# Kernel tuning notes

Measured on AMD Instinct MI355X. Metric: run time of the kernel, lower is better.

The kernel has to match this reference:

```python
import jax, jax.numpy as jnp
import numpy as np

HIDDEN = 768
NUM_HEADS = 12
HEAD_DIM = HIDDEN // NUM_HEADS
B, S = 4, 2048


def setup_inputs() -> dict:
    key = jax.random.key(0)
    ks = jax.random.split(key, 10)
    scale = 1.0 / np.sqrt(HIDDEN)
    return {
        "hidden_states": jax.random.normal(ks[0], (B, S, HIDDEN), dtype=jnp.float32),
        "attention_mask": jnp.ones((B, S), dtype=jnp.float32),
        "Wq": jax.random.normal(ks[1], (HIDDEN, HIDDEN), dtype=jnp.float32) * scale,
        "bq": jnp.zeros((HIDDEN,), dtype=jnp.float32),
        "Wk": jax.random.normal(ks[2], (HIDDEN, HIDDEN), dtype=jnp.float32) * scale,
        "bk": jnp.zeros((HIDDEN,), dtype=jnp.float32),
        "Wv": jax.random.normal(ks[3], (HIDDEN, HIDDEN), dtype=jnp.float32) * scale,
        "bv": jnp.zeros((HIDDEN,), dtype=jnp.float32),
        "Wo": jax.random.normal(ks[4], (HIDDEN, HIDDEN), dtype=jnp.float32) * scale,
        "bo": jnp.zeros((HIDDEN,), dtype=jnp.float32),
    }


def reference(hidden_states, attention_mask, Wq, bq, Wk, bk, Wv, bv, Wo, bo):
    b, s, _ = hidden_states.shape
    # nn.Linear: x @ W.T + b  (W is [out, in])
    Q = hidden_states @ Wq.T + bq
    K = hidden_states @ Wk.T + bk
    V = hidden_states @ Wv.T + bv
    # [b, s, h*d] -> [b, h, s, d]
    Q = Q.reshape(b, s, NUM_HEADS, HEAD_DIM).transpose(0, 2, 1, 3)
    K = K.reshape(b, s, NUM_HEADS, HEAD_DIM).transpose(0, 2, 1, 3)
    V = V.reshape(b, s, NUM_HEADS, HEAD_DIM).transpose(0, 2, 1, 3)
    # scores: [b, h, s, s]
    scores = jnp.einsum("bhqd,bhkd->bhqk", Q, K) / jnp.sqrt(
        jnp.asarray(HEAD_DIM, dtype=Q.dtype))
    # mask: [b, s] -> additive bias broadcast over heads and query dim
    bias = (1.0 - attention_mask)[:, None, None, :] * -10000.0
    scores = scores + bias
    probs = jax.nn.softmax(scores, axis=-1)  # dropout p=0.0 -> identity
    context = jnp.einsum("bhqk,bhkd->bhqd", probs, V)
    context = context.transpose(0, 2, 1, 3).reshape(b, s, HIDDEN)
    return context @ Wo.T + bo
```

## Files before the change

### kernel.cpp

```cpp
#include <hip/hip_runtime.h>
#include <hip/hip_bf16.h>

#define SEQ   2048
#define NH    12
#define MTOK  8192

typedef __attribute__((ext_vector_type(8))) short short8;
typedef __attribute__((ext_vector_type(4))) short short4v;
typedef __attribute__((ext_vector_type(4))) float f32x4;

__device__ inline short f2bf(float x) {
  __hip_bfloat16 h = __float2bfloat16(x);
  return *(short*)&h;
}

#define GLL(gp, lp) __builtin_amdgcn_global_load_lds( \
    (const __attribute__((address_space(1))) void*)(gp), \
    (__attribute__((address_space(3))) void*)(lp), 16, 0, 0)

#define MFMA(a, b, c) __builtin_amdgcn_mfma_f32_16x16x32_bf16(a, b, c, 0, 0, 0)

#if !defined(__HIP_DEVICE_COMPILE__)
#define MFMA16(a, b, c) (c)
#elif __has_builtin(__builtin_amdgcn_mfma_f32_16x16x16bf16_1k)
#define MFMA16(a, b, c) __builtin_amdgcn_mfma_f32_16x16x16bf16_1k(a, b, c, 0, 0, 0)
#elif __has_builtin(__builtin_amdgcn_mfma_f32_16x16x16_bf16)
#define MFMA16(a, b, c) __builtin_amdgcn_mfma_f32_16x16x16_bf16(a, b, c, 0, 0, 0)
#else
#error "no 16x16x16 bf16 mfma builtin on device"
#endif

#if !defined(__HIP_DEVICE_COMPILE__)
#define EXP2(x) (x)
#elif __has_builtin(__builtin_amdgcn_exp2f)
#define EXP2(x) __builtin_amdgcn_exp2f(x)
#else
#define EXP2(x) __expf((x) * 0.6931471805599453f)
#endif

__device__ inline unsigned pack2bf(float a, float b) {
  unsigned ua = __float_as_uint(a) + 0x8000u;
  unsigned ub = __float_as_uint(b) + 0x8000u;
#if defined(__HIP_DEVICE_COMPILE__) && __has_builtin(__builtin_amdgcn_perm)
  return __builtin_amdgcn_perm(ub, ua, 0x07060302u);
#else
  return (ub & 0xFFFF0000u) | (ua >> 16);
#endif
}

union PackFrag {
  unsigned u[2];
  short4v s;
};

#define QSCALE 0.18033688011112042f
#define MBSCALE -14426.950408889634f

__global__ __launch_bounds__(256) void prep(
    const float* __restrict__ hs, const float* __restrict__ Wq,
    const float* __restrict__ Wk, const float* __restrict__ Wv,
    const float* __restrict__ Wo, const float* __restrict__ mask,
    short* __restrict__ Xb, short* __restrict__ Wqkvb,
    short* __restrict__ Wob, float* __restrict__ mbias) {
  int bid = blockIdx.x;
  if (bid < 6144) {
    int i = bid * 256 + threadIdx.x;
    float4 v = ((const float4*)hs)[i];
    short4v o;
    o[0] = f2bf(v.x); o[1] = f2bf(v.y); o[2] = f2bf(v.z); o[3] = f2bf(v.w);
    ((short4v*)Xb)[i] = o;
  } else if (bid < 6144 + 2304) {
    int idx = (bid - 6144) * 256 + threadIdx.x;
    int r = idx / 192, c = (idx - r * 192) * 4;
    const float* src;
    short* dst;
    int rr;
    if (r < 768)       { src = Wq; rr = r;        dst = Wqkvb; }
    else if (r < 1536) { src = Wk; rr = r - 768;  dst = Wqkvb; }
    else if (r < 2304) { src = Wv; rr = r - 1536; dst = Wqkvb; }
    else               { src = Wo; rr = r - 2304; dst = Wob; r = rr; }
    float4 v = *(const float4*)&src[(size_t)rr * 768 + c];
    short4v o;
    o[0] = f2bf(v.x); o[1] = f2bf(v.y); o[2] = f2bf(v.z); o[3] = f2bf(v.w);
    *(short4v*)&dst[(size_t)r * 768 + c] = o;
  } else {
    int i = (bid - 6144 - 2304) * 256 + threadIdx.x;
    if (i < MTOK) mbias[i] = (1.f - mask[i]) * MBSCALE;
  }
}

#define GEMM_BK64_LOOP(Aptr, Bptr)                                            \
  __shared__ __align__(16) short As[128 * 64];                                \
  __shared__ __align__(16) short Bs[128 * 64];                                \
  const int t = threadIdx.x;                                                  \
  const int wid = t >> 6, lane = t & 63, l15 = lane & 15, quad = lane >> 4;   \
  const int bm = blockIdx.x * 128, bn = blockIdx.y * 128;                     \
  const int mq = (wid & 1) * 64, nq = (wid >> 1) * 64;                        \
  const int srow8 = lane >> 3;                                                \
  const int schunk = lane & 7;                                                \
  const int scol = (schunk ^ srow8) * 8;                                      \
  f32x4 acc[4][4] = {};                                                       \
  const short *gA[4], *gB[4];                                                 \
  _Pragma("unroll") for (int g = 0; g < 4; ++g) {                             \
    int row = wid * 32 + g * 8 + srow8;                                       \
    gA[g] = (Aptr) + (size_t)(bm + row) * 768 + scol;                         \
    gB[g] = (Bptr) + (size_t)(bn + row) * 768 + scol;                         \
  }                                                                           \
  for (int k0 = 0; k0 < 768; k0 += 64) {                                      \
    _Pragma("unroll") for (int g = 0; g < 4; ++g)                             \
      GLL(gA[g] + k0, &As[(wid * 32 + g * 8) * 64]);                          \
    _Pragma("unroll") for (int g = 0; g < 4; ++g)                             \
      GLL(gB[g] + k0, &Bs[(wid * 32 + g * 8) * 64]);                          \
    __syncthreads();                                                          \
    _Pragma("unroll") for (int ks = 0; ks < 2; ++ks) {                        \
      short8 a[4], b[4];                                                      \
      _Pragma("unroll") for (int mt = 0; mt < 4; ++mt)                        \
        a[mt] = *(const short8*)&As[(mq + mt * 16 + l15) * 64 +               \
                                    (((ks * 4 + quad) ^ (l15 & 7)) * 8)];     \
      _Pragma("unroll") for (int nt = 0; nt < 4; ++nt)                        \
        b[nt] = *(const short8*)&Bs[(nq + nt * 16 + l15) * 64 +               \
                                    (((ks * 4 + quad) ^ (l15 & 7)) * 8)];     \
      _Pragma("unroll") for (int mt = 0; mt < 4; ++mt)                        \
        _Pragma("unroll") for (int nt = 0; nt < 4; ++nt)                      \
          acc[mt][nt] = MFMA(a[mt], b[nt], acc[mt][nt]);                      \
    }                                                                         \
    __syncthreads();                                                          \
  }

__global__ __launch_bounds__(256) void gemm_qkv(
    const short* __restrict__ A, const short* __restrict__ B,
    const float* __restrict__ bq, const float* __restrict__ bk,
    const float* __restrict__ bv, short* __restrict__ Qb,
    short* __restrict__ Kb, short* __restrict__ Vt) {
  GEMM_BK64_LOOP(A, B)

  const int seg = bn >= 1536 ? 2 : (bn >= 768 ? 1 : 0);
  const float* bias = seg == 0 ? bq : (seg == 1 ? bk : bv);
  const int colbase = bn - seg * 768;

  if (seg < 2) {
    short* dst = seg == 0 ? Qb : Kb;
    const float sc = seg == 0 ? QSCALE : 1.f;
#pragma unroll
    for (int mt = 0; mt < 4; ++mt)
#pragma unroll
      for (int nt = 0; nt < 4; ++nt) {
        int col = colbase + nq + nt * 16 + l15;
        float bias_v = bias[col];
#pragma unroll
        for (int i = 0; i < 4; ++i) {
          int row = bm + mq + mt * 16 + quad * 4 + i;
          dst[(size_t)row * 768 + col] = f2bf((acc[mt][nt][i] + bias_v) * sc);
        }
      }
  } else {
#pragma unroll
    for (int mt = 0; mt < 4; ++mt) {
      int row0 = bm + mq + mt * 16 + quad * 4;
      int b_ = row0 >> 11, s = row0 & 2047;
#pragma unroll
      for (int nt = 0; nt < 4; ++nt) {
        int col = colbase + nq + nt * 16 + l15;
        float bias_v = bias[col];
        int h = col >> 6, d = col & 63;
        short4v pv;
#pragma unroll
        for (int i = 0; i < 4; ++i) pv[i] = f2bf(acc[mt][nt][i] + bias_v);
        *(short4v*)&Vt[(((size_t)b_ * NH + h) * 64 + d) * 2048 + s] = pv;
      }
    }
  }
}

__global__ __launch_bounds__(256) void gemm_out(
    const short* __restrict__ A, const short* __restrict__ B,
    const float* __restrict__ bias, float* __restrict__ C) {
  GEMM_BK64_LOOP(A, B)

#pragma unroll
  for (int mt = 0; mt < 4; ++mt)
#pragma unroll
    for (int nt = 0; nt < 4; ++nt) {
      int col = bn + nq + nt * 16 + l15;
      float bias_v = bias[col];
#pragma unroll
      for (int i = 0; i < 4; ++i) {
        int row = bm + mq + mt * 16 + quad * 4 + i;
        C[(size_t)row * 768 + col] = acc[mt][nt][i] + bias_v;
      }
    }
}

__global__ __launch_bounds__(256, 3) void attn_v8(
    const short* __restrict__ Qb, const short* __restrict__ Kb,
    const short* __restrict__ Vt, const float* __restrict__ maskb,
    short* __restrict__ Ctx) {
  __shared__ __align__(16) short Ks[2][64 * 64];
  __shared__ __align__(16) short Vs[2][64 * 64];
  const int t = threadIdx.x;
  const int w = t >> 6, lane = t & 63, l15 = lane & 15, quad = lane >> 4;
  const int bh = blockIdx.x, b = bh / NH, h = bh % NH;
  const int q0 = blockIdx.y * 128;

  short8 qa[2][2];
#pragma unroll
  for (int qt = 0; qt < 2; ++qt)
#pragma unroll
    for (int ks = 0; ks < 2; ++ks) {
      int row = b * 2048 + q0 + w * 32 + qt * 16 + l15;
      qa[qt][ks] = *(const short8*)&Qb[(size_t)row * 768 + h * 64 + ks * 32 + quad * 8];
    }

  f32x4 O[2][4] = {};
  f32x4 lacc[2] = {};
  short4v ones4;
#pragma unroll
  for (int j = 0; j < 4; ++j) ones4[j] = (short)0x3F80;

  const int r0 = w * 16 + (lane >> 3);
  const int pc = lane & 7;
  const int swz0 = (pc ^ (r0 & 7)) * 8;
  const int swz1 = (pc ^ ((r0 + 8) & 7)) * 8;
  const short* gK0 = Kb + (size_t)(b * 2048 + r0) * 768 + h * 64 + swz0;
  const short* gK1 = Kb + (size_t)(b * 2048 + r0 + 8) * 768 + h * 64 + swz1;
  const short* gV0 = Vt + ((size_t)bh * 64 + r0) * 2048 + swz0;
  const short* gV1 = Vt + ((size_t)bh * 64 + r0 + 8) * 2048 + swz1;
  const float* mb = maskb + b * 2048;
  const int rs = l15 & 7;

  GLL(gK0, &Ks[0][(w * 16) * 64]);
  GLL(gK1, &Ks[0][(w * 16 + 8) * 64]);
  GLL(gV0, &Vs[0][(w * 16) * 64]);
  GLL(gV1, &Vs[0][(w * 16 + 8) * 64]);

  for (int ti = 0; ti < 32; ++ti) {
    const int cur = ti & 1;
    const int k0 = ti * 64;
    __syncthreads();

    {
      const size_t kn = (size_t)(((ti + 1) & 31) * 64);
      GLL(gK0 + kn * 768, &Ks[1 - cur][(w * 16) * 64]);
      GLL(gK1 + kn * 768, &Ks[1 - cur][(w * 16 + 8) * 64]);
      GLL(gV0 + kn, &Vs[1 - cur][(w * 16) * 64]);
      GLL(gV1 + kn, &Vs[1 - cur][(w * 16 + 8) * 64]);
    }

    f32x4 S[4][2] = {};
#pragma unroll
    for (int ks = 0; ks < 2; ++ks) {
      short8 kb[4];
#pragma unroll
      for (int kt = 0; kt < 4; ++kt)
        kb[kt] = *(const short8*)&Ks[cur][(kt * 16 + l15) * 64 +
                                         (((ks * 4 + quad) ^ rs) * 8)];
#pragma unroll
      for (int kt = 0; kt < 4; ++kt) {
        S[kt][0] = MFMA(kb[kt], qa[0][ks], S[kt][0]);
        S[kt][1] = MFMA(kb[kt], qa[1][ks], S[kt][1]);
      }
    }

    short4v pb[4][2];
#pragma unroll
    for (int kt = 0; kt < 4; ++kt) {
      float4 mb4 = *(const float4*)&mb[k0 + kt * 16 + quad * 4];
#pragma unroll
      for (int qt = 0; qt < 2; ++qt) {
        float p0 = EXP2(S[kt][qt][0] + mb4.x);
        float p1 = EXP2(S[kt][qt][1] + mb4.y);
        float p2 = EXP2(S[kt][qt][2] + mb4.z);
        float p3 = EXP2(S[kt][qt][3] + mb4.w);
        PackFrag pf;
        pf.u[0] = pack2bf(p0, p1);
        pf.u[1] = pack2bf(p2, p3);
        pb[kt][qt] = pf.s;
      }
    }

#pragma unroll
    for (int kt = 0; kt < 4; ++kt) {
      lacc[0] = MFMA16(ones4, pb[kt][0], lacc[0]);
      lacc[1] = MFMA16(ones4, pb[kt][1], lacc[1]);
    }

#pragma unroll
    for (int kt = 0; kt < 4; ++kt) {
#pragma unroll
      for (int dt = 0; dt < 4; ++dt) {
        short4v av = *(const short4v*)&Vs[cur][(dt * 16 + l15) * 64 +
            (((kt * 2 + (quad >> 1)) ^ rs) * 8) + (quad & 1) * 4];
        O[0][dt] = MFMA16(av, pb[kt][0], O[0][dt]);
        O[1][dt] = MFMA16(av, pb[kt][1], O[1][dt]);
      }
    }
  }

#pragma unroll
  for (int qt = 0; qt < 2; ++qt) {
    float inv = 1.f / lacc[qt][0];
    int row = b * 2048 + q0 + w * 32 + qt * 16 + l15;
#pragma unroll
    for (int dt = 0; dt < 4; ++dt) {
      PackFrag pf;
      pf.u[0] = pack2bf(O[qt][dt][0] * inv, O[qt][dt][1] * inv);
      pf.u[1] = pack2bf(O[qt][dt][2] * inv, O[qt][dt][3] * inv);
      *(short4v*)&Ctx[(size_t)row * 768 + h * 64 + dt * 16 + quad * 4] = pf.s;
    }
  }
}

extern "C" void kernel_launch(void* const* d_in, const int* in_sizes, int n_in,
                              void* d_out, int out_size, void* d_ws,
                              size_t ws_size, hipStream_t stream) {
  const float* hs   = (const float*)d_in[0];
  const float* mask = (const float*)d_in[1];
  const float* Wq   = (const float*)d_in[2];
  const float* bq   = (const float*)d_in[3];
  const float* Wk   = (const float*)d_in[4];
  const float* bk   = (const float*)d_in[5];
  const float* Wv   = (const float*)d_in[6];
  const float* bv   = (const float*)d_in[7];
  const float* Wo   = (const float*)d_in[8];
  const float* bo   = (const float*)d_in[9];

  char* ws = (char*)d_ws;
  short* Xb    = (short*)(ws);
  short* Wqkvb = (short*)(ws + 12582912);
  short* Wob   = (short*)(ws + 16121856);
  short* Qb    = (short*)(ws + 17301504);
  short* Kb    = (short*)(ws + 29884416);
  short* Vtg   = (short*)(ws + 42467328);
  short* Ctxb  = (short*)(ws + 55050240);
  float* mbias = (float*)(ws + 67633152);

  prep<<<8480, 256, 0, stream>>>(hs, Wq, Wk, Wv, Wo, mask,
                                 Xb, Wqkvb, Wob, mbias);
  gemm_qkv<<<dim3(64, 18), 256, 0, stream>>>(Xb, Wqkvb, bq, bk, bv,
                                             Qb, Kb, Vtg);
  attn_v8<<<dim3(48, 16), 256, 0, stream>>>(Qb, Kb, Vtg, mbias, Ctxb);
  gemm_out<<<dim3(64, 6), 256, 0, stream>>>(Ctxb, Wob, bo, (float*)d_out);
}
```

Before: 229.6 us.

## Split attention block into 8 waves of 16 query rows each

Attention blocks now launch 8 waves of 512 threads. Each wave handles 16 query rows instead of 32, and each thread loads one K and one V row chunk per tile instead of two. This halves per-thread registers and work so more waves can fit per CU and hide latency. In exchange, K/V fragments read from LDS are reused across fewer query rows, so LDS read traffic per unit of MFMA work doubles.

```diff
diff --git a/kernel.cpp b/kernel.cpp
--- a/kernel.cpp
+++ b/kernel.cpp
@@ -191,7 +191,7 @@
     }
 }
 
-__global__ __launch_bounds__(256, 3) void attn_v8(
+__global__ __launch_bounds__(512, 6) void attn_v9(
     const short* __restrict__ Qb, const short* __restrict__ Kb,
     const short* __restrict__ Vt, const float* __restrict__ maskb,
     short* __restrict__ Ctx) {
@@ -202,36 +202,29 @@
   const int bh = blockIdx.x, b = bh / NH, h = bh % NH;
   const int q0 = blockIdx.y * 128;
 
-  short8 qa[2][2];
-#pragma unroll
-  for (int qt = 0; qt < 2; ++qt)
-#pragma unroll
-    for (int ks = 0; ks < 2; ++ks) {
-      int row = b * 2048 + q0 + w * 32 + qt * 16 + l15;
-      qa[qt][ks] = *(const short8*)&Qb[(size_t)row * 768 + h * 64 + ks * 32 + quad * 8];
-    }
-
-  f32x4 O[2][4] = {};
-  f32x4 lacc[2] = {};
+  short8 qa[2];
+#pragma unroll
+  for (int ks = 0; ks < 2; ++ks) {
+    int row = b * 2048 + q0 + w * 16 + l15;
+    qa[ks] = *(const short8*)&Qb[(size_t)row * 768 + h * 64 + ks * 32 + quad * 8];
+  }
+
+  f32x4 O[4] = {};
+  f32x4 lacc = {};
   short4v ones4;
 #pragma unroll
   for (int j = 0; j < 4; ++j) ones4[j] = (short)0x3F80;
 
-  const int r0 = w * 16 + (lane >> 3);
+  const int r0 = w * 8 + (lane >> 3);
   const int pc = lane & 7;
-  const int swz0 = (pc ^ (r0 & 7)) * 8;
-  const int swz1 = (pc ^ ((r0 + 8) & 7)) * 8;
-  const short* gK0 = Kb + (size_t)(b * 2048 + r0) * 768 + h * 64 + swz0;
-  const short* gK1 = Kb + (size_t)(b * 2048 + r0 + 8) * 768 + h * 64 + swz1;
-  const short* gV0 = Vt + ((size_t)bh * 64 + r0) * 2048 + swz0;
-  const short* gV1 = Vt + ((size_t)bh * 64 + r0 + 8) * 2048 + swz1;
+  const int swz = (pc ^ (r0 & 7)) * 8;
+  const short* gK = Kb + (size_t)(b * 2048 + r0) * 768 + h * 64 + swz;
+  const short* gV = Vt + ((size_t)bh * 64 + r0) * 2048 + swz;
   const float* mb = maskb + b * 2048;
   const int rs = l15 & 7;
 
-  GLL(gK0, &Ks[0][(w * 16) * 64]);
-  GLL(gK1, &Ks[0][(w * 16 + 8) * 64]);
-  GLL(gV0, &Vs[0][(w * 16) * 64]);
-  GLL(gV1, &Vs[0][(w * 16 + 8) * 64]);
+  GLL(gK, &Ks[0][(w * 8) * 64]);
+  GLL(gV, &Vs[0][(w * 8) * 64]);
 
   for (int ti = 0; ti < 32; ++ti) {
     const int cur = ti & 1;
@@ -240,13 +233,11 @@
 
     {
       const size_t kn = (size_t)(((ti + 1) & 31) * 64);
-      GLL(gK0 + kn * 768, &Ks[1 - cur][(w * 16) * 64]);
-      GLL(gK1 + kn * 768, &Ks[1 - cur][(w * 16 + 8) * 64]);
-      GLL(gV0 + kn, &Vs[1 - cur][(w * 16) * 64]);
-      GLL(gV1 + kn, &Vs[1 - cur][(w * 16 + 8) * 64]);
-    }
-
-    f32x4 S[4][2] = {};
+      GLL(gK + kn * 768, &Ks[1 - cur][(w * 8) * 64]);
+      GLL(gV + kn, &Vs[1 - cur][(w * 8) * 64]);
+    }
+
+    f32x4 S[4] = {};
 #pragma unroll
     for (int ks = 0; ks < 2; ++ks) {
       short8 kb[4];
@@ -255,34 +246,27 @@
         kb[kt] = *(const short8*)&Ks[cur][(kt * 16 + l15) * 64 +
                                          (((ks * 4 + quad) ^ rs) * 8)];
 #pragma unroll
-      for (int kt = 0; kt < 4; ++kt) {
-        S[kt][0] = MFMA(kb[kt], qa[0][ks], S[kt][0]);
-        S[kt][1] = MFMA(kb[kt], qa[1][ks], S[kt][1]);
-      }
-    }
-
-    short4v pb[4][2];
+      for (int kt = 0; kt < 4; ++kt)
+        S[kt] = MFMA(kb[kt], qa[ks], S[kt]);
+    }
+
+    short4v pb[4];
 #pragma unroll
     for (int kt = 0; kt < 4; ++kt) {
       float4 mb4 = *(const float4*)&mb[k0 + kt * 16 + quad * 4];
-#pragma unroll
-      for (int qt = 0; qt < 2; ++qt) {
-        float p0 = EXP2(S[kt][qt][0] + mb4.x);
-        float p1 = EXP2(S[kt][qt][1] + mb4.y);
-        float p2 = EXP2(S[kt][qt][2] + mb4.z);
-        float p3 = EXP2(S[kt][qt][3] + mb4.w);
-        PackFrag pf;
-        pf.u[0] = pack2bf(p0, p1);
-        pf.u[1] = pack2bf(p2, p3);
-        pb[kt][qt] = pf.s;
-      }
-    }
-
-#pragma unroll
-    for (int kt = 0; kt < 4; ++kt) {
-      lacc[0] = MFMA16(ones4, pb[kt][0], lacc[0]);
-      lacc[1] = MFMA16(ones4, pb[kt][1], lacc[1]);
-    }
+      float p0 = EXP2(S[kt][0] + mb4.x);
+      float p1 = EXP2(S[kt][1] + mb4.y);
+      float p2 = EXP2(S[kt][2] + mb4.z);
+      float p3 = EXP2(S[kt][3] + mb4.w);
+      PackFrag pf;
+      pf.u[0] = pack2bf(p0, p1);
+      pf.u[1] = pack2bf(p2, p3);
+      pb[kt] = pf.s;
+    }
+
+#pragma unroll
+    for (int kt = 0; kt < 4; ++kt)
+      lacc = MFMA16(ones4, pb[kt], lacc);
 
 #pragma unroll
     for (int kt = 0; kt < 4; ++kt) {
@@ -290,21 +274,19 @@
       for (int dt = 0; dt < 4; ++dt) {
         short4v av = *(const short4v*)&Vs[cur][(dt * 16 + l15) * 64 +
             (((kt * 2 + (quad >> 1)) ^ rs) * 8) + (quad & 1) * 4];
-        O[0][dt] = MFMA16(av, pb[kt][0], O[0][dt]);
-        O[1][dt] = MFMA16(av, pb[kt][1], O[1][dt]);
+        O[dt] = MFMA16(av, pb[kt], O[dt]);
       }
     }
   }
 
-#pragma unroll
-  for (int qt = 0; qt < 2; ++qt) {
-    float inv = 1.f / lacc[qt][0];
-    int row = b * 2048 + q0 + w * 32 + qt * 16 + l15;
+  {
+    float inv = 1.f / lacc[0];
+    int row = b * 2048 + q0 + w * 16 + l15;
 #pragma unroll
     for (int dt = 0; dt < 4; ++dt) {
       PackFrag pf;
-      pf.u[0] = pack2bf(O[qt][dt][0] * inv, O[qt][dt][1] * inv);
-      pf.u[1] = pack2bf(O[qt][dt][2] * inv, O[qt][dt][3] * inv);
+      pf.u[0] = pack2bf(O[dt][0] * inv, O[dt][1] * inv);
+      pf.u[1] = pack2bf(O[dt][2] * inv, O[dt][3] * inv);
       *(short4v*)&Ctx[(size_t)row * 768 + h * 64 + dt * 16 + quad * 4] = pf.s;
     }
   }
@@ -338,6 +320,6 @@
                                  Xb, Wqkvb, Wob, mbias);
   gemm_qkv<<<dim3(64, 18), 256, 0, stream>>>(Xb, Wqkvb, bq, bk, bv,
                                              Qb, Kb, Vtg);
-  attn_v8<<<dim3(48, 16), 256, 0, stream>>>(Qb, Kb, Vtg, mbias, Ctxb);
+  attn_v9<<<dim3(48, 16), 512, 0, stream>>>(Qb, Kb, Vtg, mbias, Ctxb);
   gemm_out<<<dim3(64, 6), 256, 0, stream>>>(Ctxb, Wob, bo, (float*)d_out);
 }
```

Measured after the change: 236.4 us. +3.0%, slower.
